# Kernel optimization log

Hardware: AMD Instinct MI355X
Metric: run time of the kernel (lower is better)

The kernel has to match this reference:

```python
import jax, jax.numpy as jnp
import numpy as np

T, B, F = 160, 640, 40          # time-major input [T, B, F]
H, PJ, L = 768, 256, 3          # nb_hidden, nb_proj, nb_layers
FORGET_BIAS = 1.0               # TF LSTMCell default


def _glorot(k, shape):
    std = (2.0 / (shape[0] + shape[1])) ** 0.5
    return jax.random.normal(k, shape, jnp.float32) * std


def setup_inputs() -> dict:
    key = jax.random.key(0)
    ks = jax.random.split(key, 7)
    x = jax.random.normal(ks[0], (T, B, F), jnp.float32)
    # layer 0: input dim F + proj state PJ; layers 1,2: input dim PJ + PJ
    W0 = _glorot(ks[1], (F + PJ, 4 * H)); b0 = jnp.zeros((4 * H,), jnp.float32)
    P0 = _glorot(ks[2], (H, PJ))
    W1 = _glorot(ks[3], (PJ + PJ, 4 * H)); b1 = jnp.zeros((4 * H,), jnp.float32)
    P1 = _glorot(ks[4], (H, PJ))
    W2 = _glorot(ks[5], (PJ + PJ, 4 * H)); b2 = jnp.zeros((4 * H,), jnp.float32)
    P2 = _glorot(ks[6], (H, PJ))
    return {"x": x, "W0": W0, "b0": b0, "P0": P0,
            "W1": W1, "b1": b1, "P1": P1,
            "W2": W2, "b2": b2, "P2": P2}


def _cell(xt, c, h, W, b, P):
    # TF LSTMCell with num_proj: gates on [x, m_prev]; gate order i, j, f, o.
    z = jnp.concatenate([xt, h], axis=-1) @ W + b            # [B, 4H]
    i, j, f, o = jnp.split(z, 4, axis=-1)
    c_new = jax.nn.sigmoid(f + FORGET_BIAS) * c + jax.nn.sigmoid(i) * jnp.tanh(j)
    m = jax.nn.sigmoid(o) * jnp.tanh(c_new)                  # [B, H]
    h_new = m @ P                                            # projected state [B, PJ]
    return c_new, h_new


def reference(x, W0, b0, P0, W1, b1, P1, W2, b2, P2):
    params = ((W0, b0, P0), (W1, b1, P1), (W2, b2, P2))
    Bd = x.shape[1]
    init = tuple((jnp.zeros((Bd, H), x.dtype), jnp.zeros((Bd, PJ), x.dtype))
                 for _ in range(L))

    def step(carry, xt):
        inp = xt
        new = []
        for (c, h), (W, b, P) in zip(carry, params):
            c, h = _cell(inp, c, h, W, b, P)
            new.append((c, h))
            inp = h
        return tuple(new), None

    carry, _ = jax.lax.scan(step, init, x)
    emb = carry[-1][1]                                       # last layer h at final step, [B, PJ]
    # tf.nn.l2_normalize
    return emb / jnp.sqrt(jnp.maximum(jnp.sum(emb * emb, axis=-1, keepdims=True), 1e-12))
```

## Files before the change

### kernel.cpp

```cpp
#include <hip/hip_runtime.h>
#include <hip/hip_cooperative_groups.h>

namespace cg = cooperative_groups;

#define Bdim 640
#define Hdim 768
#define PJdim 256
#define Tdim 160
#define NSTEP (Tdim + 2)

typedef _Float16 half8 __attribute__((ext_vector_type(8)));
typedef float floatx4 __attribute__((ext_vector_type(4)));

constexpr size_t HB_HALFS = 3ull * Bdim * PJdim;
constexpr size_t ZP_OFF   = HB_HALFS * 2;
constexpr size_t MB_OFF   = ZP_OFF + 256;
constexpr size_t MB_HALFS = 3ull * Bdim * Hdim;
constexpr size_t X_OFF    = MB_OFF + MB_HALFS * 2;
constexpr size_t X_HALFS  = (size_t)Tdim * Bdim * 40;
constexpr size_t W_OFF    = X_OFF + X_HALFS * 2;
constexpr size_t W_HALFS  = 36ull * 131072;
constexpr size_t P_OFF    = W_OFF + W_HALFS * 2;
constexpr size_t P_HALFS  = 3ull * 196608;
constexpr size_t C_OFF    = P_OFF + P_HALFS * 2;
constexpr size_t C_BYTES  = 3ull * Bdim * Hdim * 4;

__device__ __forceinline__ float sigm(float v) { return 1.0f / (1.0f + __expf(-v)); }
__device__ __forceinline__ float tanh_fast(float v) { return 2.0f / (1.0f + __expf(-2.0f * v)) - 1.0f; }

__global__ void repack_kernel(const float* __restrict__ x,
                              const float* __restrict__ W0, const float* __restrict__ W1,
                              const float* __restrict__ W2, const float* __restrict__ P0,
                              const float* __restrict__ P1, const float* __restrict__ P2,
                              _Float16* __restrict__ Wfrag, _Float16* __restrict__ Pfrag,
                              _Float16* __restrict__ x16)
{
    size_t idx = (size_t)blockIdx.x * 256 + threadIdx.x;
    if (idx < W_HALFS) {
        int slab = (int)(idx >> 17);
        int l = slab / 12, ht = slab % 12;
        int r  = (int)(idx & 131071);
        int kc = r >> 13;
        int r2 = r & 8191;
        int g  = r2 >> 11;
        int cf = (r2 >> 9) & 3;
        int u  = r2 & 511;
        int lane = u >> 3, e = u & 7;
        int qd = lane >> 4, ln = lane & 15;
        int k   = kc * 32 + qd * 8 + e;
        int col = g * Hdim + ht * 64 + cf * 16 + ln;
        float v;
        if (l == 0)      v = (k < 296) ? W0[(size_t)k * 3072 + col] : 0.0f;
        else if (l == 1) v = W1[(size_t)k * 3072 + col];
        else             v = W2[(size_t)k * 3072 + col];
        Wfrag[idx] = (_Float16)v;
    } else if (idx < W_HALFS + P_HALFS) {
        size_t i = idx - W_HALFS;
        int l = (int)(i / 196608);
        int r = (int)(i % 196608);
        int cq = r / 49152;
        int r2 = r % 49152;
        int kc = r2 / 2048;
        int r3 = r2 & 2047;
        int cg = r3 >> 9;
        int u  = r3 & 511;
        int lane = u >> 3, e = u & 7;
        int qd = lane >> 4, ln = lane & 15;
        int k  = kc * 32 + qd * 8 + e;
        int pj = cq * 64 + cg * 16 + ln;
        const float* P = (l == 0) ? P0 : (l == 1) ? P1 : P2;
        Pfrag[i] = (_Float16)P[(size_t)k * PJdim + pj];
    } else if (idx < W_HALFS + P_HALFS + X_HALFS) {
        size_t i = idx - W_HALFS - P_HALFS;
        x16[i] = (_Float16)x[i];
    }
}

__device__ __forceinline__ void gate_step(
    int l, int b0r, int h0, int KC, int t,
    const half8 (&Breg)[16][2], float (&c)[8][2],
    const float (&bia)[2], const float (&bja)[2], const float (&bfa)[2], const float (&boa)[2],
    const _Float16* __restrict__ x16, const _Float16* __restrict__ h16,
    const _Float16* __restrict__ zerop, _Float16* __restrict__ mbuf,
    _Float16* __restrict__ Ast, float* __restrict__ zst, int tid)
{
    const int wv = tid >> 6, lane = tid & 63, qd = lane >> 4, ln = lane & 15;
    const int g = wv >> 1, hh = wv & 1;
    const int qd8 = qd * 8;
    const int rowg = b0r + wv * 16 + ln;

    const _Float16* xt  = x16 + ((size_t)t * Bdim + rowg) * 40;
    const _Float16* h0b = h16 + (size_t)rowg * PJdim - 40;
    const _Float16* lob = (l > 0) ? h16 + ((size_t)(l - 1) * Bdim + rowg) * PJdim : nullptr;
    const _Float16* hib = h16 + ((size_t)l * Bdim + rowg) * PJdim - 256;

    auto srcp = [&](int kc) -> const _Float16* {
        int k = kc * 32 + qd8;
        if (l == 0) return (k < 40) ? xt + k : (k < 296) ? h0b + k : zerop;
        return (k < 256) ? lob + k : hib + k;
    };

    floatx4 acc[8][2];
    const floatx4 fz = {0.f, 0.f, 0.f, 0.f};
#pragma unroll
    for (int i = 0; i < 8; ++i) { acc[i][0] = fz; acc[i][1] = fz; }

    uint4 pre = *(const uint4*)srcp(0);
#pragma unroll
    for (int kc = 0; kc < 16; ++kc) {
        if (kc < KC) {
            *(uint4*)(Ast + (size_t)(kc & 1) * 4096 + wv * 512 + lane * 8) = pre;
            if (kc + 1 < KC) pre = *(const uint4*)srcp(kc + 1);
            __syncthreads();
            const _Float16* Ab = Ast + (size_t)(kc & 1) * 4096;
#pragma unroll
            for (int rf = 0; rf < 8; ++rf) {
                half8 af = *(const half8*)(Ab + rf * 512 + lane * 8);
                acc[rf][0] = __builtin_amdgcn_mfma_f32_16x16x32_f16(af, Breg[kc][0], acc[rf][0], 0, 0, 0);
                acc[rf][1] = __builtin_amdgcn_mfma_f32_16x16x32_f16(af, Breg[kc][1], acc[rf][1], 0, 0, 0);
            }
        }
    }

    const int trow = tid >> 5;
    const int hc0  = (tid * 2) & 63;
#pragma unroll
    for (int rf = 0; rf < 8; ++rf) {
        __syncthreads();
#pragma unroll
        for (int cf = 0; cf < 2; ++cf)
#pragma unroll
            for (int r = 0; r < 4; ++r)
                zst[(qd * 4 + r) * 256 + g * 64 + hh * 32 + cf * 16 + ln] = acc[rf][cf][r];
        __syncthreads();
        _Float16 mh[2];
#pragma unroll
        for (int j = 0; j < 2; ++j) {
            int hc = hc0 + j;
            float zi = zst[trow * 256 + hc]       + bia[j];
            float zj = zst[trow * 256 + 64 + hc]  + bja[j];
            float zf = zst[trow * 256 + 128 + hc] + bfa[j];
            float zo = zst[trow * 256 + 192 + hc] + boa[j];
            float cn = sigm(zf) * c[rf][j] + sigm(zi) * tanh_fast(zj);
            c[rf][j] = cn;
            mh[j] = (_Float16)(sigm(zo) * tanh_fast(cn));
        }
        union { _Float16 h2[2]; unsigned u; } pk;
        pk.h2[0] = mh[0]; pk.h2[1] = mh[1];
        int row_g = b0r + rf * 16 + trow;
        *(unsigned*)(mbuf + ((size_t)l * Bdim + row_g) * Hdim + h0 + hc0) = pk.u;
    }
}

__device__ __forceinline__ void proj_step(
    int l, int b0r, int cq, const half8 (&Preg)[24],
    const _Float16* __restrict__ mbuf, _Float16* __restrict__ h16,
    _Float16* __restrict__ Ast, int tid)
{
    const int wv = tid >> 6, lane = tid & 63, qd = lane >> 4, ln = lane & 15;
    const int rh = wv >> 2, cg = wv & 3;
    const int rowg = b0r + wv * 16 + ln;
    const _Float16* mrow = mbuf + ((size_t)l * Bdim + rowg) * Hdim + qd * 8;

    floatx4 pacc[4];
    const floatx4 fz = {0.f, 0.f, 0.f, 0.f};
#pragma unroll
    for (int i = 0; i < 4; ++i) pacc[i] = fz;

    uint4 pre = *(const uint4*)(mrow);
#pragma unroll
    for (int kc = 0; kc < 24; ++kc) {
        *(uint4*)(Ast + (size_t)(kc & 1) * 4096 + wv * 512 + lane * 8) = pre;
        if (kc < 23) pre = *(const uint4*)(mrow + (kc + 1) * 32);
        __syncthreads();
        const _Float16* Ab = Ast + (size_t)(kc & 1) * 4096;
#pragma unroll
        for (int rfl = 0; rfl < 4; ++rfl) {
            half8 af = *(const half8*)(Ab + (rh * 4 + rfl) * 512 + lane * 8);
            pacc[rfl] = __builtin_amdgcn_mfma_f32_16x16x32_f16(af, Preg[kc], pacc[rfl], 0, 0, 0);
        }
        __syncthreads();
    }
#pragma unroll
    for (int rfl = 0; rfl < 4; ++rfl)
#pragma unroll
        for (int r = 0; r < 4; ++r) {
            int row = b0r + (rh * 4 + rfl) * 16 + qd * 4 + r;
            h16[((size_t)l * Bdim + row) * PJdim + cq * 64 + cg * 16 + ln] = (_Float16)pacc[rfl][r];
        }
}

__device__ __forceinline__ void load_Breg(const _Float16* __restrict__ Wfrag, int l, int ht,
                                          int wv, int lane, half8 (&Breg)[16][2])
{
    const int g = wv >> 1, hh = wv & 1;
    const _Float16* wslab = Wfrag + ((size_t)(l * 12 + ht)) * 131072;
#pragma unroll
    for (int kc = 0; kc < 16; ++kc)
#pragma unroll
        for (int cf = 0; cf < 2; ++cf)
            Breg[kc][cf] = *(const half8*)(wslab + kc * 8192 + g * 2048 + (hh * 2 + cf) * 512 + lane * 8);
}

__device__ __forceinline__ void load_Preg(const _Float16* __restrict__ Pfrag, int l, int cq,
                                          int wv, int lane, half8 (&Preg)[24])
{
    const int cg = wv & 3;
    const _Float16* pslab = Pfrag + (size_t)l * 196608 + (size_t)cq * 49152;
#pragma unroll
    for (int kc = 0; kc < 24; ++kc)
        Preg[kc] = *(const half8*)(pslab + kc * 2048 + cg * 512 + lane * 8);
}

__device__ __forceinline__ void load_bias(const float* __restrict__ bias, int h0, int tid,
                                          float (&bia)[2], float (&bja)[2], float (&bfa)[2], float (&boa)[2])
{
    int hcg = h0 + ((tid * 2) & 63);
#pragma unroll
    for (int j = 0; j < 2; ++j) {
        bia[j] = bias[hcg + j];
        bja[j] = bias[Hdim + hcg + j];
        bfa[j] = bias[2 * Hdim + hcg + j] + 1.0f;
        boa[j] = bias[3 * Hdim + hcg + j];
    }
}

__device__ __forceinline__ void finalize_row(const _Float16* __restrict__ h16,
                                             float* __restrict__ out, int row, int lane)
{
    const _Float16* e = h16 + ((size_t)2 * Bdim + row) * PJdim + lane * 4;
    float v0 = (float)e[0], v1 = (float)e[1], v2 = (float)e[2], v3 = (float)e[3];
    float ss = v0 * v0 + v1 * v1 + v2 * v2 + v3 * v3;
#pragma unroll
    for (int o = 32; o > 0; o >>= 1) ss += __shfl_xor(ss, o, 64);
    float rs = rsqrtf(fmaxf(ss, 1e-12f));
    float4 o4; o4.x = v0 * rs; o4.y = v1 * rs; o4.z = v2 * rs; o4.w = v3 * rs;
    *(float4*)(out + (size_t)row * PJdim + lane * 4) = o4;
}

__global__ __launch_bounds__(512)
void lstm_persist(const _Float16* __restrict__ x16, const _Float16* __restrict__ Wfrag,
                  const _Float16* __restrict__ Pfrag,
                  const float* __restrict__ bias0, const float* __restrict__ bias1,
                  const float* __restrict__ bias2,
                  _Float16* __restrict__ h16, _Float16* __restrict__ mbuf,
                  const _Float16* __restrict__ zerop, float* __restrict__ out)
{
    cg::grid_group grid = cg::this_grid();
    __shared__ __align__(16) _Float16 Ast[2 * 4096];
    __shared__ __align__(16) float zst[16 * 256];

    const int tid = threadIdx.x, bid = blockIdx.x;
    const int wv = tid >> 6, lane = tid & 63;

    const int xcd = bid & 7, slot = bid >> 3;
    const int gid = xcd * 2 + (slot >> 4);
    const int rr  = slot & 15;
    const bool active = (gid < 15);
    const int bt2 = active ? gid / 3 : 0;
    const int l   = active ? gid % 3 : 0;
    const bool isgate = active && (rr < 12);
    const bool isproj = active && (rr >= 12);
    const int b0r = bt2 * 128;

    if (isgate) {
        const int ht = rr, h0 = ht * 64;
        const int KC = (l == 0) ? 10 : 16;
        half8 Breg[16][2];
        load_Breg(Wfrag, l, ht, wv, lane, Breg);
        float bia[2], bja[2], bfa[2], boa[2];
        load_bias((l == 0) ? bias0 : (l == 1) ? bias1 : bias2, h0, tid, bia, bja, bfa, boa);
        float c[8][2];
#pragma unroll
        for (int i = 0; i < 8; ++i) { c[i][0] = 0.f; c[i][1] = 0.f; }
        for (int s = 0; s < NSTEP; ++s) {
            const int t = s - l;
            if (t >= 0 && t < Tdim)
                gate_step(l, b0r, h0, KC, t, Breg, c, bia, bja, bfa, boa,
                          x16, h16, zerop, mbuf, Ast, zst, tid);
            grid.sync();
            grid.sync();
        }
    } else if (isproj) {
        const int cq = rr - 12;
        half8 Preg[24];
        load_Preg(Pfrag, l, cq, wv, lane, Preg);
        for (int s = 0; s < NSTEP; ++s) {
            grid.sync();
            const int tp = s - l;
            if (tp >= 0 && tp < Tdim)
                proj_step(l, b0r, cq, Preg, mbuf, h16, Ast, tid);
            grid.sync();
        }
    } else {
        for (int s = 0; s < NSTEP; ++s) { grid.sync(); grid.sync(); }
    }

    if (bid < 80) {
        int row = bid * 8 + wv;
        finalize_row(h16, out, row, lane);
    }
}

__global__ __launch_bounds__(512)
void gate_fb(const _Float16* __restrict__ x16, const _Float16* __restrict__ Wfrag,
             const float* __restrict__ bias0, const float* __restrict__ bias1,
             const float* __restrict__ bias2,
             _Float16* __restrict__ h16, _Float16* __restrict__ mbuf,
             const _Float16* __restrict__ zerop, float* __restrict__ cfb, int s)
{
    __shared__ __align__(16) _Float16 Ast[2 * 4096];
    __shared__ __align__(16) float zst[16 * 256];
    const int tid = threadIdx.x, bid = blockIdx.x;
    const int ht = bid % 12, z = bid / 12, l = z % 3, bt2 = z / 3;
    const int t = s - l;
    if (t < 0 || t >= Tdim) return;
    const int wv = tid >> 6, lane = tid & 63;
    const int b0r = bt2 * 128, h0 = ht * 64;
    const int KC = (l == 0) ? 10 : 16;
    half8 Breg[16][2];
    load_Breg(Wfrag, l, ht, wv, lane, Breg);
    float bia[2], bja[2], bfa[2], boa[2];
    load_bias((l == 0) ? bias0 : (l == 1) ? bias1 : bias2, h0, tid, bia, bja, bfa, boa);
    const int trow = tid >> 5, hc0 = (tid * 2) & 63;
    float c[8][2];
#pragma unroll
    for (int rf = 0; rf < 8; ++rf)
#pragma unroll
        for (int j = 0; j < 2; ++j)
            c[rf][j] = cfb[((size_t)l * Bdim + b0r + rf * 16 + trow) * Hdim + h0 + hc0 + j];
    gate_step(l, b0r, h0, KC, t, Breg, c, bia, bja, bfa, boa, x16, h16, zerop, mbuf, Ast, zst, tid);
#pragma unroll
    for (int rf = 0; rf < 8; ++rf)
#pragma unroll
        for (int j = 0; j < 2; ++j)
            cfb[((size_t)l * Bdim + b0r + rf * 16 + trow) * Hdim + h0 + hc0 + j] = c[rf][j];
}

__global__ __launch_bounds__(512)
void proj_fb(const _Float16* __restrict__ Pfrag, const _Float16* __restrict__ mbuf,
             _Float16* __restrict__ h16, int s)
{
    __shared__ __align__(16) _Float16 Ast[2 * 4096];
    const int tid = threadIdx.x, bid = blockIdx.x;
    const int cq = bid & 3, z = bid >> 2, l = z % 3, bt2 = z / 3;
    const int tp = s - l;
    if (tp < 0 || tp >= Tdim) return;
    const int wv = tid >> 6, lane = tid & 63;
    half8 Preg[24];
    load_Preg(Pfrag, l, cq, wv, lane, Preg);
    proj_step(l, bt2 * 128, cq, Preg, mbuf, h16, Ast, tid);
}

__global__ __launch_bounds__(512)
void fin_fb(const _Float16* __restrict__ h16, float* __restrict__ out)
{
    int row = blockIdx.x * 8 + (threadIdx.x >> 6);
    finalize_row(h16, out, row, threadIdx.x & 63);
}

extern "C" void kernel_launch(void* const* d_in, const int* in_sizes, int n_in,
                              void* d_out, int out_size, void* d_ws, size_t ws_size,
                              hipStream_t stream)
{
    (void)in_sizes; (void)n_in; (void)out_size; (void)ws_size;
    const float* x  = (const float*)d_in[0];
    const float* W0 = (const float*)d_in[1];
    const float* b0 = (const float*)d_in[2];
    const float* P0 = (const float*)d_in[3];
    const float* W1 = (const float*)d_in[4];
    const float* b1 = (const float*)d_in[5];
    const float* P1 = (const float*)d_in[6];
    const float* W2 = (const float*)d_in[7];
    const float* b2 = (const float*)d_in[8];
    const float* P2 = (const float*)d_in[9];

    char* ws = (char*)d_ws;
    _Float16* h16   = (_Float16*)(ws);
    _Float16* zerop = (_Float16*)(ws + ZP_OFF);
    _Float16* mbuf  = (_Float16*)(ws + MB_OFF);
    _Float16* x16   = (_Float16*)(ws + X_OFF);
    _Float16* Wfrag = (_Float16*)(ws + W_OFF);
    _Float16* Pfrag = (_Float16*)(ws + P_OFF);
    float*    cfb   = (float*)(ws + C_OFF);
    float*    outp  = (float*)d_out;

    hipMemsetAsync(ws, 0, ZP_OFF + 256, stream);
    hipMemsetAsync(cfb, 0, C_BYTES, stream);

    {
        constexpr size_t total = W_HALFS + P_HALFS + X_HALFS;
        int grid = (int)((total + 255) / 256);
        repack_kernel<<<grid, 256, 0, stream>>>(x, W0, W1, W2, P0, P1, P2, Wfrag, Pfrag, x16);
    }

    int occ = 0;
    hipError_t oe = hipOccupancyMaxActiveBlocksPerMultiprocessor(&occ, lstm_persist, 512, 0);
    bool coop = (oe == hipSuccess && occ >= 1);
    if (coop) {
        void* args[] = { (void*)&x16, (void*)&Wfrag, (void*)&Pfrag,
                         (void*)&b0, (void*)&b1, (void*)&b2,
                         (void*)&h16, (void*)&mbuf, (void*)&zerop, (void*)&outp };
        hipError_t le = hipLaunchCooperativeKernel((const void*)lstm_persist,
                                                   dim3(256), dim3(512), args, 0, stream);
        if (le != hipSuccess) { (void)hipGetLastError(); coop = false; }
    }
    if (!coop) {
        for (int s = 0; s < NSTEP; ++s) {
            gate_fb<<<180, 512, 0, stream>>>(x16, Wfrag, b0, b1, b2, h16, mbuf, zerop, cfb, s);
            proj_fb<<<60, 512, 0, stream>>>(Pfrag, mbuf, h16, s);
        }
        fin_fb<<<80, 512, 0, stream>>>(h16, outp);
    }
}
```

Baseline: 5.143 ms.

## Replace grid-wide syncs with per-group dataflow counters and double K-chunk staging

The persistent LSTM kernel drops cooperative grid.sync barriers in favour of per-group atomic counters. Gate blocks wait only on their own layer's projection and the lower layer's projection, and projection blocks wait on gates, so layers and batch tiles can pipeline as a wavefront. The final normalisation moves into layer-2 gate blocks. The gate and projection GEMM loops also stage two K-chunks per LDS barrier, which halves the syncthreads count and doubles LDS use. The risks are spin-wait overhead, memory-ordering subtleties from relaxed atomics plus fences, and the flags aliasing the cfb region.

```diff
diff --git a/kernel.cpp b/kernel.cpp
--- a/kernel.cpp
+++ b/kernel.cpp
@@ -1,7 +1,4 @@
 #include <hip/hip_runtime.h>
-#include <hip/hip_cooperative_groups.h>
-
-namespace cg = cooperative_groups;
 
 #define Bdim 640
 #define Hdim 768
@@ -27,6 +24,29 @@
 
 __device__ __forceinline__ float sigm(float v) { return 1.0f / (1.0f + __expf(-v)); }
 __device__ __forceinline__ float tanh_fast(float v) { return 2.0f / (1.0f + __expf(-2.0f * v)) - 1.0f; }
+
+__device__ __forceinline__ void pipe_wait(unsigned* c0, unsigned t0, unsigned* c1, unsigned t1)
+{
+    if (threadIdx.x == 0) {
+        if (t0)
+            while (__hip_atomic_load(c0, __ATOMIC_RELAXED, __HIP_MEMORY_SCOPE_AGENT) < t0)
+                __builtin_amdgcn_s_sleep(1);
+        if (c1 && t1)
+            while (__hip_atomic_load(c1, __ATOMIC_RELAXED, __HIP_MEMORY_SCOPE_AGENT) < t1)
+                __builtin_amdgcn_s_sleep(1);
+        __threadfence();
+    }
+    __syncthreads();
+}
+
+__device__ __forceinline__ void pipe_sig(unsigned* c)
+{
+    __syncthreads();
+    if (threadIdx.x == 0) {
+        __threadfence();
+        __hip_atomic_fetch_add(c, 1u, __ATOMIC_RELAXED, __HIP_MEMORY_SCOPE_AGENT);
+    }
+}
 
 __global__ void repack_kernel(const float* __restrict__ x,
                               const float* __restrict__ W0, const float* __restrict__ W1,
@@ -62,12 +82,12 @@
         int r2 = r % 49152;
         int kc = r2 / 2048;
         int r3 = r2 & 2047;
-        int cg = r3 >> 9;
+        int cgr = r3 >> 9;
         int u  = r3 & 511;
         int lane = u >> 3, e = u & 7;
         int qd = lane >> 4, ln = lane & 15;
         int k  = kc * 32 + qd * 8 + e;
-        int pj = cq * 64 + cg * 16 + ln;
+        int pj = cq * 64 + cgr * 16 + ln;
         const float* P = (l == 0) ? P0 : (l == 1) ? P1 : P2;
         Pfrag[i] = (_Float16)P[(size_t)k * PJdim + pj];
     } else if (idx < W_HALFS + P_HALFS + X_HALFS) {
@@ -105,20 +125,29 @@
 #pragma unroll
     for (int i = 0; i < 8; ++i) { acc[i][0] = fz; acc[i][1] = fz; }
 
-    uint4 pre = *(const uint4*)srcp(0);
-#pragma unroll
-    for (int kc = 0; kc < 16; ++kc) {
-        if (kc < KC) {
-            *(uint4*)(Ast + (size_t)(kc & 1) * 4096 + wv * 512 + lane * 8) = pre;
-            if (kc + 1 < KC) pre = *(const uint4*)srcp(kc + 1);
+    const int CH = KC >> 1;
+    uint4 pre0 = *(const uint4*)srcp(0);
+    uint4 pre1 = *(const uint4*)srcp(1);
+#pragma unroll
+    for (int ch = 0; ch < 8; ++ch) {
+        if (ch < CH) {
+            _Float16* Aw = Ast + (size_t)(ch & 1) * 8192 + wv * 512 + lane * 8;
+            *(uint4*)Aw          = pre0;
+            *(uint4*)(Aw + 4096) = pre1;
+            if (ch + 1 < CH) {
+                pre0 = *(const uint4*)srcp(2 * ch + 2);
+                pre1 = *(const uint4*)srcp(2 * ch + 3);
+            }
             __syncthreads();
-            const _Float16* Ab = Ast + (size_t)(kc & 1) * 4096;
-#pragma unroll
-            for (int rf = 0; rf < 8; ++rf) {
-                half8 af = *(const half8*)(Ab + rf * 512 + lane * 8);
-                acc[rf][0] = __builtin_amdgcn_mfma_f32_16x16x32_f16(af, Breg[kc][0], acc[rf][0], 0, 0, 0);
-                acc[rf][1] = __builtin_amdgcn_mfma_f32_16x16x32_f16(af, Breg[kc][1], acc[rf][1], 0, 0, 0);
-            }
+            const _Float16* Ab = Ast + (size_t)(ch & 1) * 8192;
+#pragma unroll
+            for (int sub = 0; sub < 2; ++sub)
+#pragma unroll
+                for (int rf = 0; rf < 8; ++rf) {
+                    half8 af = *(const half8*)(Ab + sub * 4096 + rf * 512 + lane * 8);
+                    acc[rf][0] = __builtin_amdgcn_mfma_f32_16x16x32_f16(af, Breg[2 * ch + sub][0], acc[rf][0], 0, 0, 0);
+                    acc[rf][1] = __builtin_amdgcn_mfma_f32_16x16x32_f16(af, Breg[2 * ch + sub][1], acc[rf][1], 0, 0, 0);
+                }
         }
     }
 
@@ -158,7 +187,7 @@
     _Float16* __restrict__ Ast, int tid)
 {
     const int wv = tid >> 6, lane = tid & 63, qd = lane >> 4, ln = lane & 15;
-    const int rh = wv >> 2, cg = wv & 3;
+    const int rh = wv >> 2, cgi = wv & 3;
     const int rowg = b0r + wv * 16 + ln;
     const _Float16* mrow = mbuf + ((size_t)l * Bdim + rowg) * Hdim + qd * 8;
 
@@ -167,26 +196,33 @@
 #pragma unroll
     for (int i = 0; i < 4; ++i) pacc[i] = fz;
 
-    uint4 pre = *(const uint4*)(mrow);
-#pragma unroll
-    for (int kc = 0; kc < 24; ++kc) {
-        *(uint4*)(Ast + (size_t)(kc & 1) * 4096 + wv * 512 + lane * 8) = pre;
-        if (kc < 23) pre = *(const uint4*)(mrow + (kc + 1) * 32);
+    uint4 pre0 = *(const uint4*)(mrow);
+    uint4 pre1 = *(const uint4*)(mrow + 32);
+#pragma unroll
+    for (int ch = 0; ch < 12; ++ch) {
+        _Float16* Aw = Ast + (size_t)(ch & 1) * 8192 + wv * 512 + lane * 8;
+        *(uint4*)Aw          = pre0;
+        *(uint4*)(Aw + 4096) = pre1;
+        if (ch < 11) {
+            pre0 = *(const uint4*)(mrow + (2 * ch + 2) * 32);
+            pre1 = *(const uint4*)(mrow + (2 * ch + 3) * 32);
+        }
         __syncthreads();
-        const _Float16* Ab = Ast + (size_t)(kc & 1) * 4096;
-#pragma unroll
-        for (int rfl = 0; rfl < 4; ++rfl) {
-            half8 af = *(const half8*)(Ab + (rh * 4 + rfl) * 512 + lane * 8);
-            pacc[rfl] = __builtin_amdgcn_mfma_f32_16x16x32_f16(af, Preg[kc], pacc[rfl], 0, 0, 0);
-        }
-        __syncthreads();
+        const _Float16* Ab = Ast + (size_t)(ch & 1) * 8192;
+#pragma unroll
+        for (int sub = 0; sub < 2; ++sub)
+#pragma unroll
+            for (int rfl = 0; rfl < 4; ++rfl) {
+                half8 af = *(const half8*)(Ab + sub * 4096 + (rh * 4 + rfl) * 512 + lane * 8);
+                pacc[rfl] = __builtin_amdgcn_mfma_f32_16x16x32_f16(af, Preg[2 * ch + sub], pacc[rfl], 0, 0, 0);
+            }
     }
 #pragma unroll
     for (int rfl = 0; rfl < 4; ++rfl)
 #pragma unroll
         for (int r = 0; r < 4; ++r) {
             int row = b0r + (rh * 4 + rfl) * 16 + qd * 4 + r;
-            h16[((size_t)l * Bdim + row) * PJdim + cq * 64 + cg * 16 + ln] = (_Float16)pacc[rfl][r];
+            h16[((size_t)l * Bdim + row) * PJdim + cq * 64 + cgi * 16 + ln] = (_Float16)pacc[rfl][r];
         }
 }
 
@@ -205,11 +241,11 @@
 __device__ __forceinline__ void load_Preg(const _Float16* __restrict__ Pfrag, int l, int cq,
                                           int wv, int lane, half8 (&Preg)[24])
 {
-    const int cg = wv & 3;
+    const int cgi = wv & 3;
     const _Float16* pslab = Pfrag + (size_t)l * 196608 + (size_t)cq * 49152;
 #pragma unroll
     for (int kc = 0; kc < 24; ++kc)
-        Preg[kc] = *(const half8*)(pslab + kc * 2048 + cg * 512 + lane * 8);
+        Preg[kc] = *(const half8*)(pslab + kc * 2048 + cgi * 512 + lane * 8);
 }
 
 __device__ __forceinline__ void load_bias(const float* __restrict__ bias, int h0, int tid,
@@ -244,10 +280,10 @@
                   const float* __restrict__ bias0, const float* __restrict__ bias1,
                   const float* __restrict__ bias2,
                   _Float16* __restrict__ h16, _Float16* __restrict__ mbuf,
-                  const _Float16* __restrict__ zerop, float* __restrict__ out)
-{
-    cg::grid_group grid = cg::this_grid();
-    __shared__ __align__(16) _Float16 Ast[2 * 4096];
+                  const _Float16* __restrict__ zerop, float* __restrict__ out,
+                  unsigned* __restrict__ flags)
+{
+    __shared__ __align__(16) _Float16 Ast[2 * 8192];
     __shared__ __align__(16) float zst[16 * 256];
 
     const int tid = threadIdx.x, bid = blockIdx.x;
@@ -256,14 +292,14 @@
     const int xcd = bid & 7, slot = bid >> 3;
     const int gid = xcd * 2 + (slot >> 4);
     const int rr  = slot & 15;
-    const bool active = (gid < 15);
-    const int bt2 = active ? gid / 3 : 0;
-    const int l   = active ? gid % 3 : 0;
-    const bool isgate = active && (rr < 12);
-    const bool isproj = active && (rr >= 12);
+    if (gid >= 15) return;
+    const int bt2 = gid / 3, l = gid % 3;
     const int b0r = bt2 * 128;
 
-    if (isgate) {
+    unsigned* gd = flags + (size_t)gid * 64;
+    unsigned* pd = gd + 32;
+
+    if (rr < 12) {
         const int ht = rr, h0 = ht * 64;
         const int KC = (l == 0) ? 10 : 16;
         half8 Breg[16][2];
@@ -273,32 +309,29 @@
         float c[8][2];
 #pragma unroll
         for (int i = 0; i < 8; ++i) { c[i][0] = 0.f; c[i][1] = 0.f; }
-        for (int s = 0; s < NSTEP; ++s) {
-            const int t = s - l;
-            if (t >= 0 && t < Tdim)
-                gate_step(l, b0r, h0, KC, t, Breg, c, bia, bja, bfa, boa,
-                          x16, h16, zerop, mbuf, Ast, zst, tid);
-            grid.sync();
-            grid.sync();
-        }
-    } else if (isproj) {
+        unsigned* pd_lo = (l > 0) ? flags + (size_t)(gid - 1) * 64 + 32 : nullptr;
+        for (int t = 0; t < Tdim; ++t) {
+            pipe_wait(pd, 4u * (unsigned)t, pd_lo, (l > 0) ? 4u * (unsigned)(t + 1) : 0u);
+            gate_step(l, b0r, h0, KC, t, Breg, c, bia, bja, bfa, boa,
+                      x16, h16, zerop, mbuf, Ast, zst, tid);
+            pipe_sig(gd);
+        }
+        if (l == 2 && rr < 8) {
+            pipe_wait(pd, 4u * (unsigned)Tdim, nullptr, 0u);
+            int row0 = b0r + rr * 16 + wv * 2;
+            finalize_row(h16, out, row0, lane);
+            finalize_row(h16, out, row0 + 1, lane);
+        }
+    } else {
         const int cq = rr - 12;
         half8 Preg[24];
         load_Preg(Pfrag, l, cq, wv, lane, Preg);
-        for (int s = 0; s < NSTEP; ++s) {
-            grid.sync();
-            const int tp = s - l;
-            if (tp >= 0 && tp < Tdim)
-                proj_step(l, b0r, cq, Preg, mbuf, h16, Ast, tid);
-            grid.sync();
-        }
-    } else {
-        for (int s = 0; s < NSTEP; ++s) { grid.sync(); grid.sync(); }
-    }
-
-    if (bid < 80) {
-        int row = bid * 8 + wv;
-        finalize_row(h16, out, row, lane);
+        unsigned* gd_hi = (l < 2) ? flags + (size_t)(gid + 1) * 64 : nullptr;
+        for (int t = 0; t < Tdim; ++t) {
+            pipe_wait(gd, 12u * (unsigned)(t + 1), gd_hi, (l < 2) ? 12u * (unsigned)t : 0u);
+            proj_step(l, b0r, cq, Preg, mbuf, h16, Ast, tid);
+            pipe_sig(pd);
+        }
     }
 }
 
@@ -309,7 +342,7 @@
              _Float16* __restrict__ h16, _Float16* __restrict__ mbuf,
              const _Float16* __restrict__ zerop, float* __restrict__ cfb, int s)
 {
-    __shared__ __align__(16) _Float16 Ast[2 * 4096];
+    __shared__ __align__(16) _Float16 Ast[2 * 8192];
     __shared__ __align__(16) float zst[16 * 256];
     const int tid = threadIdx.x, bid = blockIdx.x;
     const int ht = bid % 12, z = bid / 12, l = z % 3, bt2 = z / 3;
@@ -341,7 +374,7 @@
 void proj_fb(const _Float16* __restrict__ Pfrag, const _Float16* __restrict__ mbuf,
              _Float16* __restrict__ h16, int s)
 {
-    __shared__ __align__(16) _Float16 Ast[2 * 4096];
+    __shared__ __align__(16) _Float16 Ast[2 * 8192];
     const int tid = threadIdx.x, bid = blockIdx.x;
     const int cq = bid & 3, z = bid >> 2, l = z % 3, bt2 = z / 3;
     const int tp = s - l;
@@ -383,6 +416,7 @@
     _Float16* Wfrag = (_Float16*)(ws + W_OFF);
     _Float16* Pfrag = (_Float16*)(ws + P_OFF);
     float*    cfb   = (float*)(ws + C_OFF);
+    unsigned* flags = (unsigned*)(ws + C_OFF);
     float*    outp  = (float*)d_out;
 
     hipMemsetAsync(ws, 0, ZP_OFF + 256, stream);
@@ -400,7 +434,8 @@
     if (coop) {
         void* args[] = { (void*)&x16, (void*)&Wfrag, (void*)&Pfrag,
                          (void*)&b0, (void*)&b1, (void*)&b2,
-                         (void*)&h16, (void*)&mbuf, (void*)&zerop, (void*)&outp };
+                         (void*)&h16, (void*)&mbuf, (void*)&zerop, (void*)&outp,
+                         (void*)&flags };
         hipError_t le = hipLaunchCooperativeKernel((const void*)lstm_persist,
                                                    dim3(256), dim3(512), args, 0, stream);
         if (le != hipSuccess) { (void)hipGetLastError(); coop = false; }
```

Result: faster. 4.839 ms (-5.9%).
